# Optimization experiments

Measured on AMD Instinct MI355X. Metric: run time of the kernel, lower is better.

The kernel has to match this reference:

```python
import jax, jax.numpy as jnp
import numpy as np

N = 100000
E = 3200000
IN_DIM = 256
HID = 64
OUT = 40


def setup_inputs() -> dict:
    key = jax.random.key(0)
    ks = jax.random.split(key, 8)
    x = jax.random.normal(ks[0], (N, IN_DIM), dtype=jnp.float32)
    edge_index = jax.random.randint(ks[1], (2, E), 0, N, dtype=jnp.int64)
    # Glorot-ish init for weights
    W1 = jax.random.normal(ks[2], (IN_DIM, HID), dtype=jnp.float32) / np.sqrt(IN_DIM)
    b1 = jnp.zeros((HID,), dtype=jnp.float32)
    W2 = jax.random.normal(ks[3], (HID, HID), dtype=jnp.float32) / np.sqrt(HID)
    b2 = jnp.zeros((HID,), dtype=jnp.float32)
    W3 = jax.random.normal(ks[4], (HID, OUT), dtype=jnp.float32) / np.sqrt(HID)
    b3 = jax.random.normal(ks[5], (OUT,), dtype=jnp.float32) * 0.01
    return {"x": x, "edge_index": edge_index,
            "W1": W1, "b1": b1, "W2": W2, "b2": b2, "W3": W3, "b3": b3}


def _gcn_norm(edge_index, n):
    # Add self-loops, compute symmetric normalization deg^-1/2 A deg^-1/2
    loop = jnp.arange(n, dtype=edge_index.dtype)
    src = jnp.concatenate([edge_index[0], loop])
    dst = jnp.concatenate([edge_index[1], loop])
    deg = jax.ops.segment_sum(jnp.ones_like(dst, dtype=jnp.float32), dst,
                              num_segments=n)
    dinv = jnp.where(deg > 0, jax.lax.rsqrt(deg), 0.0)
    norm = dinv[src] * dinv[dst]  # [E+N]
    return src, dst, norm


def _gcn_conv(x, src, dst, norm, W, b, n):
    h = x @ W                                  # transform first (small dim)
    msg = h[src] * norm[:, None]               # gather + scale
    out = jax.ops.segment_sum(msg, dst, num_segments=n)  # scatter-add
    return out + b


def reference(x, edge_index, W1, b1, W2, b2, W3, b3):
    n = x.shape[0]
    src, dst, norm = _gcn_norm(edge_index, n)
    h = jax.nn.relu(_gcn_conv(x, src, dst, norm, W1, b1, n))
    h = jax.nn.relu(_gcn_conv(h, src, dst, norm, W2, b2, n))
    logits = h @ W3 + b3
    return jax.nn.log_softmax(logits, axis=1)
```

## Files before the change

kernel.cpp:

```cpp
#include <hip/hip_runtime.h>
#include <hip/hip_fp16.h>
#include <cstdint>


constexpr int CHUNK = 8192;
constexpr int BKCAP = 8192;

__global__ __launch_bounds__(256) void p2_localsort(
        const int* __restrict__ esrc, const int* __restrict__ edst, int E,
        unsigned* __restrict__ pairs1, int* __restrict__ cntMat,
        int* __restrict__ startMat, int NBK) {
    __shared__ int hist[1024];
    __shared__ int wsum[256];
    __shared__ unsigned lp[CHUNK];
    const int t = threadIdx.x, blk = blockIdx.x;
    const int base = blk * CHUNK;
    const int cnt = min(CHUNK, E - base);
    for (int i = t; i < 1024; i += 256) hist[i] = 0;
    __syncthreads();
    for (int i = t; i < cnt; i += 256) atomicAdd(&hist[edst[base + i] >> 7], 1);
    __syncthreads();
    int h0 = hist[4*t], h1 = hist[4*t+1], h2 = hist[4*t+2], h3 = hist[4*t+3];
    int s = h0 + h1 + h2 + h3;
    wsum[t] = s; __syncthreads();
    #pragma unroll
    for (int o = 1; o < 256; o <<= 1) {
        int x = (t >= o) ? wsum[t - o] : 0;
        __syncthreads(); wsum[t] += x; __syncthreads();
    }
    int run = wsum[t] - s;
    int e0 = run, e1 = run + h0, e2 = e1 + h1, e3 = e2 + h2;
    hist[4*t] = e0; hist[4*t+1] = e1; hist[4*t+2] = e2; hist[4*t+3] = e3;
    if (4*t     < NBK) { cntMat[(size_t)blk*NBK + 4*t]     = h0; startMat[(size_t)blk*NBK + 4*t]     = e0; }
    if (4*t + 1 < NBK) { cntMat[(size_t)blk*NBK + 4*t + 1] = h1; startMat[(size_t)blk*NBK + 4*t + 1] = e1; }
    if (4*t + 2 < NBK) { cntMat[(size_t)blk*NBK + 4*t + 2] = h2; startMat[(size_t)blk*NBK + 4*t + 2] = e2; }
    if (4*t + 3 < NBK) { cntMat[(size_t)blk*NBK + 4*t + 3] = h3; startMat[(size_t)blk*NBK + 4*t + 3] = e3; }
    __syncthreads();
    for (int i = t; i < cnt; i += 256) {
        int d = edst[base + i];
        int pos = atomicAdd(&hist[d >> 7], 1);
        lp[pos] = ((unsigned)(d & 127) << 17) | (unsigned)esrc[base + i];
    }
    __syncthreads();
    for (int i = t; i < cnt; i += 256) pairs1[base + i] = lp[i];
}

__global__ __launch_bounds__(256) void p3_colscan(int* __restrict__ cntMat,
        int* __restrict__ TB, int nchunks, int NBK) {
    __shared__ int buf[512];
    const int t = threadIdx.x, b = blockIdx.x;
    int v0 = (t < nchunks) ? cntMat[(size_t)t*NBK + b] : 0;
    int v1 = (t + 256 < nchunks) ? cntMat[(size_t)(t + 256)*NBK + b] : 0;
    buf[t] = v0; buf[t + 256] = v1; __syncthreads();
    #pragma unroll
    for (int o = 1; o < 512; o <<= 1) {
        int x0 = (t >= o) ? buf[t - o] : 0;
        int x1 = (t + 256 >= o) ? buf[t + 256 - o] : 0;
        __syncthreads(); buf[t] += x0; buf[t + 256] += x1; __syncthreads();
    }
    if (t < nchunks) cntMat[(size_t)t*NBK + b] = buf[t] - v0;
    if (t + 256 < nchunks) cntMat[(size_t)(t + 256)*NBK + b] = buf[t + 256] - v1;
    if (t == 0) TB[b] = buf[511];
}

__global__ __launch_bounds__(256) void p4_scan(const int* __restrict__ TB,
        int* __restrict__ bucketBase, int NBK, int E) {
    __shared__ int buf[1024];
    __shared__ int wsum[256];
    const int t = threadIdx.x;
    for (int i = t; i < 1024; i += 256) buf[i] = (i < NBK) ? TB[i] : 0;
    __syncthreads();
    int h0 = buf[4*t], h1 = buf[4*t+1], h2 = buf[4*t+2], h3 = buf[4*t+3];
    int s = h0 + h1 + h2 + h3;
    wsum[t] = s; __syncthreads();
    #pragma unroll
    for (int o = 1; o < 256; o <<= 1) {
        int x = (t >= o) ? wsum[t - o] : 0;
        __syncthreads(); wsum[t] += x; __syncthreads();
    }
    int run = wsum[t] - s;
    int e0 = run, e1 = run + h0, e2 = e1 + h1, e3 = e2 + h2;
    if (4*t     < NBK) bucketBase[4*t]     = e0;
    if (4*t + 1 < NBK) bucketBase[4*t + 1] = e1;
    if (4*t + 2 < NBK) bucketBase[4*t + 2] = e2;
    if (4*t + 3 < NBK) bucketBase[4*t + 3] = e3;
    if (t == 0) bucketBase[NBK] = E;
}

__global__ __launch_bounds__(256) void p6_sortcsr(
        const unsigned* __restrict__ pairs1, const int* __restrict__ cumMat,
        const int* __restrict__ startMat, const int* __restrict__ TB,
        const int* __restrict__ bucketBase, int nchunks, int NBK,
        int* __restrict__ csrc, int* __restrict__ rofs,
        float* __restrict__ dinv, int N, int E) {
    __shared__ unsigned lp[BKCAP];
    __shared__ int ccum[512];
    __shared__ int cstart[512];
    __shared__ int hist[128];
    __shared__ int sc[128];
    __shared__ int foffs[128];
    const int t = threadIdx.x, b = blockIdx.x;
    const int total0 = TB[b];
    const int total = min(total0, BKCAP);
    const int base = bucketBase[b];
    for (int i = t; i < nchunks; i += 256) {
        ccum[i]   = cumMat[(size_t)i * NBK + b];
        cstart[i] = startMat[(size_t)i * NBK + b];
    }
    if (t < 128) hist[t] = 0;
    if (t == 0) ccum[nchunks] = total0;
    __syncthreads();
    for (int i = t; i < total; i += 256) {
        int lo = 0, hi = nchunks - 1;
        while (lo < hi) {
            int mid = (lo + hi + 1) >> 1;
            if (ccum[mid] <= i) lo = mid; else hi = mid - 1;
        }
        unsigned v = pairs1[(size_t)lo * CHUNK + cstart[lo] + (i - ccum[lo])];
        lp[i] = v;
        atomicAdd(&hist[v >> 17], 1);
    }
    __syncthreads();
    if (t < 128) sc[t] = hist[t];
    __syncthreads();
    #pragma unroll
    for (int o = 1; o < 128; o <<= 1) {
        int x = (t >= o && t < 128) ? sc[t - o] : 0;
        __syncthreads();
        if (t < 128) sc[t] += x;
        __syncthreads();
    }
    if (t < 128) {
        int excl = sc[t] - hist[t];
        foffs[t] = excl;
        int node = b * 128 + t;
        if (node < N) {
            rofs[node] = base + excl;
            dinv[node] = rsqrtf((float)hist[t] + 1.0f);
        }
    }
    if (b == 0 && t == 255) rofs[N] = E;
    __syncthreads();
    for (int i = t; i < total; i += 256) {
        unsigned v = lp[i];
        int pos = atomicAdd(&foffs[v >> 17], 1);
        csrc[base + pos] = (int)(v & 0x1FFFFu);
    }
}

template<int K>
__global__ __launch_bounds__(256) void k_gemm(const float* __restrict__ X,
        const float* __restrict__ Wm, const float* __restrict__ dinv,
        __half* __restrict__ G, int nrows) {
    constexpr int BK = 32;
    constexpr int NCH = K / BK;
    constexpr int PITCH = 132;
    __shared__ float Xs[BK * PITCH];
    __shared__ float Ws[BK * 64];
    const int t = threadIdx.x;
    const int cg = t & 7;
    const int rg = t >> 3;
    const int brow = blockIdx.x * 128;

    float acc[4][8];
    #pragma unroll
    for (int r = 0; r < 4; ++r)
        #pragma unroll
        for (int c = 0; c < 8; ++c) acc[r][c] = 0.f;

    for (int ch = 0; ch < NCH; ++ch) {
        if (ch) __syncthreads();
        #pragma unroll
        for (int i = 0; i < 4; ++i) {
            int f = t + i * 256;
            int r = f >> 3, c4 = f & 7;
            int gr = brow + r;
            float4 v = make_float4(0.f, 0.f, 0.f, 0.f);
            if (gr < nrows)
                v = *(const float4*)(X + (size_t)gr * K + ch * BK + c4 * 4);
            Xs[(c4 * 4 + 0) * PITCH + r] = v.x;
            Xs[(c4 * 4 + 1) * PITCH + r] = v.y;
            Xs[(c4 * 4 + 2) * PITCH + r] = v.z;
            Xs[(c4 * 4 + 3) * PITCH + r] = v.w;
        }
        #pragma unroll
        for (int i = 0; i < 2; ++i) {
            int f = t + i * 256;
            int k = f >> 4, c4 = f & 15;
            *(float4*)(Ws + k * 64 + c4 * 4) =
                *(const float4*)(Wm + (size_t)(ch * BK + k) * 64 + c4 * 4);
        }
        __syncthreads();

        #pragma unroll
        for (int k = 0; k < BK; ++k) {
            float4 xa = *(const float4*)(Xs + k * PITCH + rg * 4);
            float4 w0 = *(const float4*)(Ws + k * 64 + cg * 8);
            float4 w1 = *(const float4*)(Ws + k * 64 + cg * 8 + 4);
#define FMA_ROW(r, xv) \
            acc[r][0] += (xv) * w0.x; acc[r][1] += (xv) * w0.y; \
            acc[r][2] += (xv) * w0.z; acc[r][3] += (xv) * w0.w; \
            acc[r][4] += (xv) * w1.x; acc[r][5] += (xv) * w1.y; \
            acc[r][6] += (xv) * w1.z; acc[r][7] += (xv) * w1.w;
            FMA_ROW(0, xa.x) FMA_ROW(1, xa.y) FMA_ROW(2, xa.z) FMA_ROW(3, xa.w)
#undef FMA_ROW
        }
    }
    #pragma unroll
    for (int r = 0; r < 4; ++r) {
        int gr = brow + rg * 4 + r;
        if (gr < nrows) {
            float dv = dinv[gr];
            __half2 h01 = __floats2half2_rn(acc[r][0] * dv, acc[r][1] * dv);
            __half2 h23 = __floats2half2_rn(acc[r][2] * dv, acc[r][3] * dv);
            __half2 h45 = __floats2half2_rn(acc[r][4] * dv, acc[r][5] * dv);
            __half2 h67 = __floats2half2_rn(acc[r][6] * dv, acc[r][7] * dv);
            uint4 pk;
            pk.x = *(unsigned*)&h01; pk.y = *(unsigned*)&h23;
            pk.z = *(unsigned*)&h45; pk.w = *(unsigned*)&h67;
            *(uint4*)(G + (size_t)gr * 64 + cg * 8) = pk;
        }
    }
}

#define ACC8(A0, A1, V) { \
    float2 f0_ = __half22float2(*(const __half2*)&(V).x); \
    float2 f1_ = __half22float2(*(const __half2*)&(V).y); \
    float2 f2_ = __half22float2(*(const __half2*)&(V).z); \
    float2 f3_ = __half22float2(*(const __half2*)&(V).w); \
    (A0).x += f0_.x; (A0).y += f0_.y; (A0).z += f1_.x; (A0).w += f1_.y; \
    (A1).x += f2_.x; (A1).y += f2_.y; (A1).z += f3_.x; (A1).w += f3_.y; }

__global__ __launch_bounds__(256) void k_agg(const __half* __restrict__ G,
        const int* __restrict__ rofs, const int* __restrict__ csrc,
        const float* __restrict__ dinv, const float* __restrict__ bias,
        float* __restrict__ H, int nrows) {
    const int l = threadIdx.x & 63;
    const int g = l >> 3;
    const int p = l & 7;
    const int d = blockIdx.x * 4 + (threadIdx.x >> 6);
    if (d >= nrows) return;
    const int beg = rofs[d], end = rofs[d + 1];
    float4 a0 = make_float4(0.f, 0.f, 0.f, 0.f);
    float4 a1 = make_float4(0.f, 0.f, 0.f, 0.f);

    int e = beg + g;
    for (; e + 8 < end; e += 16) {
        int s0 = csrc[e];
        int s1 = csrc[e + 8];
        uint4 v0 = *(const uint4*)(G + (size_t)s0 * 64 + p * 8);
        uint4 v1 = *(const uint4*)(G + (size_t)s1 * 64 + p * 8);
        ACC8(a0, a1, v0)
        ACC8(a0, a1, v1)
    }
    if (e < end) {
        int s = csrc[e];
        uint4 v = *(const uint4*)(G + (size_t)s * 64 + p * 8);
        ACC8(a0, a1, v)
    }
    #pragma unroll
    for (int off = 8; off <= 32; off <<= 1) {
        a0.x += __shfl_xor(a0.x, off); a0.y += __shfl_xor(a0.y, off);
        a0.z += __shfl_xor(a0.z, off); a0.w += __shfl_xor(a0.w, off);
        a1.x += __shfl_xor(a1.x, off); a1.y += __shfl_xor(a1.y, off);
        a1.z += __shfl_xor(a1.z, off); a1.w += __shfl_xor(a1.w, off);
    }
    if (g == 0) {
        uint4 sv = *(const uint4*)(G + (size_t)d * 64 + p * 8);
        float2 s0 = __half22float2(*(const __half2*)&sv.x);
        float2 s1 = __half22float2(*(const __half2*)&sv.y);
        float2 s2 = __half22float2(*(const __half2*)&sv.z);
        float2 s3 = __half22float2(*(const __half2*)&sv.w);
        const float dv = dinv[d];
        const float4* B4 = (const float4*)bias;
        float4 b0 = B4[p * 2], b1 = B4[p * 2 + 1];
        float4 o0, o1;
        o0.x = fmaxf((a0.x + s0.x) * dv + b0.x, 0.f);
        o0.y = fmaxf((a0.y + s0.y) * dv + b0.y, 0.f);
        o0.z = fmaxf((a0.z + s1.x) * dv + b0.z, 0.f);
        o0.w = fmaxf((a0.w + s1.y) * dv + b0.w, 0.f);
        o1.x = fmaxf((a1.x + s2.x) * dv + b1.x, 0.f);
        o1.y = fmaxf((a1.y + s2.y) * dv + b1.y, 0.f);
        o1.z = fmaxf((a1.z + s3.x) * dv + b1.z, 0.f);
        o1.w = fmaxf((a1.w + s3.y) * dv + b1.w, 0.f);
        float4* H4 = (float4*)(H + (size_t)d * 64 + p * 8);
        H4[0] = o0; H4[1] = o1;
    }
}

__global__ __launch_bounds__(256) void k_final(const float* __restrict__ H,
        const float* __restrict__ W3, const float* __restrict__ b3,
        float* __restrict__ out, int nrows) {
    constexpr int HP = 68;
    constexpr int OP = 44;
    __shared__ float wl[64 * 40];
    __shared__ float bl[40];
    __shared__ float Hs[256 * HP];
    const int t = threadIdx.x;
    for (int i = t; i < 640; i += 256)
        ((float4*)wl)[i] = ((const float4*)W3)[i];
    if (t < 40) bl[t] = b3[t];
    const int brow = blockIdx.x * 256;
    const int rows = min(256, nrows - brow);
    for (int i = t; i < rows * 16; i += 256) {
        int r = i >> 4, c = i & 15;
        float4 v = ((const float4*)(H + (size_t)(brow + r) * 64))[c];
        *(float4*)&Hs[r * HP + c * 4] = v;
    }
    __syncthreads();

    float acc[40];
    float lse = 0.f;
    if (t < rows) {
        #pragma unroll
        for (int j = 0; j < 40; ++j) acc[j] = bl[j];
        #pragma unroll
        for (int k4 = 0; k4 < 16; ++k4) {
            float4 h4 = *(const float4*)&Hs[t * HP + k4 * 4];
            float hv[4] = {h4.x, h4.y, h4.z, h4.w};
            #pragma unroll
            for (int c = 0; c < 4; ++c) {
                const float4* wr = (const float4*)(wl + (k4 * 4 + c) * 40);
                #pragma unroll
                for (int j4 = 0; j4 < 10; ++j4) {
                    float4 wv = wr[j4];
                    acc[j4 * 4 + 0] += hv[c] * wv.x;
                    acc[j4 * 4 + 1] += hv[c] * wv.y;
                    acc[j4 * 4 + 2] += hv[c] * wv.z;
                    acc[j4 * 4 + 3] += hv[c] * wv.w;
                }
            }
        }
        float m = acc[0];
        #pragma unroll
        for (int j = 1; j < 40; ++j) m = fmaxf(m, acc[j]);
        float s = 0.f;
        #pragma unroll
        for (int j = 0; j < 40; ++j) s += expf(acc[j] - m);
        lse = m + logf(s);
    }
    __syncthreads();
    float* Os = Hs;
    if (t < rows) {
        #pragma unroll
        for (int j4 = 0; j4 < 10; ++j4)
            *(float4*)&Os[t * OP + j4 * 4] =
                make_float4(acc[j4 * 4 + 0] - lse, acc[j4 * 4 + 1] - lse,
                            acc[j4 * 4 + 2] - lse, acc[j4 * 4 + 3] - lse);
    }
    __syncthreads();
    for (int i = t; i < rows * 40; i += 256) {
        int r = i / 40, c = i - r * 40;
        out[(size_t)brow * 40 + i] = Os[r * OP + c];
    }
}

extern "C" void kernel_launch(void* const* d_in, const int* in_sizes, int n_in,
                              void* d_out, int out_size, void* d_ws, size_t ws_size,
                              hipStream_t stream) {
    const float* x  = (const float*)d_in[0];
    const int*   ei = (const int*)d_in[1];
    const float* W1 = (const float*)d_in[2];
    const float* b1 = (const float*)d_in[3];
    const float* W2 = (const float*)d_in[4];
    const float* b2 = (const float*)d_in[5];
    const float* W3 = (const float*)d_in[6];
    const float* b3 = (const float*)d_in[7];
    float* out = (float*)d_out;

    const int HID = in_sizes[3];
    const int IND = in_sizes[2] / HID;
    const int N   = in_sizes[0] / IND;
    const int E   = in_sizes[1] / 2;
    (void)HID; (void)n_in; (void)out_size; (void)ws_size;

    const int NBK     = (N + 127) >> 7;
    const int nchunks = (E + CHUNK - 1) / CHUNK;

    char* ws = (char*)d_ws;
    size_t off = 0;
    auto alloc = [&](size_t bytes) -> char* {
        char* p = ws + off;
        off = (off + bytes + 255) & ~(size_t)255;
        return p;
    };
    size_t gbytes = (size_t)N * 64 * 2;
    size_t p1bytes = (size_t)E * 4;
    int*      cntMat     = (int*)     alloc((size_t)nchunks * NBK * 4);
    int*      startMat   = (int*)     alloc((size_t)nchunks * NBK * 4);
    int*      TB         = (int*)     alloc((size_t)NBK * 4);
    int*      bucketBase = (int*)     alloc(((size_t)NBK + 1) * 4);
    float*    dinv       = (float*)   alloc((size_t)N * 4);
    int*      rofs       = (int*)     alloc(((size_t)N + 1) * 4);
    int*      csrc       = (int*)     alloc((size_t)E * 4);
    __half*   g          = (__half*)  alloc(gbytes > p1bytes ? gbytes : p1bytes);
    float*    h          = (float*)   alloc((size_t)N * 64 * 4);
    unsigned* pairs1     = (unsigned*)g;

    const int* esrc = ei;
    const int* edst = ei + E;
    const int gM = (N + 127) / 128;
    const int gN = (N + 255) / 256;

    p2_localsort<<<nchunks, 256, 0, stream>>>(esrc, edst, E, pairs1, cntMat, startMat, NBK);
    p3_colscan  <<<NBK, 256, 0, stream>>>(cntMat, TB, nchunks, NBK);
    p4_scan     <<<1, 256, 0, stream>>>(TB, bucketBase, NBK, E);
    p6_sortcsr  <<<NBK, 256, 0, stream>>>(pairs1, cntMat, startMat, TB, bucketBase,
                                          nchunks, NBK, csrc, rofs, dinv, N, E);

    k_gemm<256> <<<gM, 256, 0, stream>>>(x, W1, dinv, g, N);
    k_agg       <<<(N + 3) / 4, 256, 0, stream>>>(g, rofs, csrc, dinv, b1, h, N);
    k_gemm<64>  <<<gM, 256, 0, stream>>>(h, W2, dinv, g, N);
    k_agg       <<<(N + 3) / 4, 256, 0, stream>>>(g, rofs, csrc, dinv, b2, h, N);
    k_final     <<<gN, 256, 0, stream>>>(h, W3, b3, out, N);
}
```

Baseline: 291.8 us.

## Restructure GEMM tile to 512 threads, 2 rows per thread, row-major LDS

Reworks the node-feature GEMM to use 512-thread blocks, each thread computing 2 rows by 8 columns instead of 4 by 8. The K chunk grows from 32 to 64, and X is stored row-major in LDS with a 65-float pitch instead of being transposed. The aim is more waves for latency hiding, fewer barriers per chunk and cheaper LDS stores. In exchange there is less register reuse per thread (2 rows per W load) and scalar LDS reads of X in place of float4 loads.

Result: slower. 306.2 us (+4.9%).

```diff
diff --git a/kernel.cpp b/kernel.cpp
--- a/kernel.cpp
+++ b/kernel.cpp
@@ -149,22 +149,22 @@
 }
 
 template<int K>
-__global__ __launch_bounds__(256) void k_gemm(const float* __restrict__ X,
+__global__ __launch_bounds__(512) void k_gemm(const float* __restrict__ X,
         const float* __restrict__ Wm, const float* __restrict__ dinv,
         __half* __restrict__ G, int nrows) {
-    constexpr int BK = 32;
+    constexpr int BK = 64;
     constexpr int NCH = K / BK;
-    constexpr int PITCH = 132;
-    __shared__ float Xs[BK * PITCH];
+    constexpr int XP = 65;
+    __shared__ float Xs[128 * XP];
     __shared__ float Ws[BK * 64];
     const int t = threadIdx.x;
     const int cg = t & 7;
     const int rg = t >> 3;
     const int brow = blockIdx.x * 128;
 
-    float acc[4][8];
-    #pragma unroll
-    for (int r = 0; r < 4; ++r)
+    float acc[2][8];
+    #pragma unroll
+    for (int r = 0; r < 2; ++r)
         #pragma unroll
         for (int c = 0; c < 8; ++c) acc[r][c] = 0.f;
 
@@ -172,43 +172,45 @@
         if (ch) __syncthreads();
         #pragma unroll
         for (int i = 0; i < 4; ++i) {
-            int f = t + i * 256;
-            int r = f >> 3, c4 = f & 7;
+            int f = t + i * 512;
+            int r = f >> 4, c4 = f & 15;
             int gr = brow + r;
             float4 v = make_float4(0.f, 0.f, 0.f, 0.f);
             if (gr < nrows)
                 v = *(const float4*)(X + (size_t)gr * K + ch * BK + c4 * 4);
-            Xs[(c4 * 4 + 0) * PITCH + r] = v.x;
-            Xs[(c4 * 4 + 1) * PITCH + r] = v.y;
-            Xs[(c4 * 4 + 2) * PITCH + r] = v.z;
-            Xs[(c4 * 4 + 3) * PITCH + r] = v.w;
+            float* xr = Xs + r * XP + c4 * 4;
+            xr[0] = v.x; xr[1] = v.y; xr[2] = v.z; xr[3] = v.w;
         }
         #pragma unroll
         for (int i = 0; i < 2; ++i) {
-            int f = t + i * 256;
+            int f = t + i * 512;
             int k = f >> 4, c4 = f & 15;
             *(float4*)(Ws + k * 64 + c4 * 4) =
                 *(const float4*)(Wm + (size_t)(ch * BK + k) * 64 + c4 * 4);
         }
         __syncthreads();
 
-        #pragma unroll
+        const float* x0p = Xs + (rg * 2 + 0) * XP;
+        const float* x1p = Xs + (rg * 2 + 1) * XP;
+        #pragma unroll 8
         for (int k = 0; k < BK; ++k) {
-            float4 xa = *(const float4*)(Xs + k * PITCH + rg * 4);
+            float x0 = x0p[k];
+            float x1 = x1p[k];
             float4 w0 = *(const float4*)(Ws + k * 64 + cg * 8);
             float4 w1 = *(const float4*)(Ws + k * 64 + cg * 8 + 4);
-#define FMA_ROW(r, xv) \
-            acc[r][0] += (xv) * w0.x; acc[r][1] += (xv) * w0.y; \
-            acc[r][2] += (xv) * w0.z; acc[r][3] += (xv) * w0.w; \
-            acc[r][4] += (xv) * w1.x; acc[r][5] += (xv) * w1.y; \
-            acc[r][6] += (xv) * w1.z; acc[r][7] += (xv) * w1.w;
-            FMA_ROW(0, xa.x) FMA_ROW(1, xa.y) FMA_ROW(2, xa.z) FMA_ROW(3, xa.w)
-#undef FMA_ROW
-        }
-    }
-    #pragma unroll
-    for (int r = 0; r < 4; ++r) {
-        int gr = brow + rg * 4 + r;
+            acc[0][0] += x0 * w0.x; acc[0][1] += x0 * w0.y;
+            acc[0][2] += x0 * w0.z; acc[0][3] += x0 * w0.w;
+            acc[0][4] += x0 * w1.x; acc[0][5] += x0 * w1.y;
+            acc[0][6] += x0 * w1.z; acc[0][7] += x0 * w1.w;
+            acc[1][0] += x1 * w0.x; acc[1][1] += x1 * w0.y;
+            acc[1][2] += x1 * w0.z; acc[1][3] += x1 * w0.w;
+            acc[1][4] += x1 * w1.x; acc[1][5] += x1 * w1.y;
+            acc[1][6] += x1 * w1.z; acc[1][7] += x1 * w1.w;
+        }
+    }
+    #pragma unroll
+    for (int r = 0; r < 2; ++r) {
+        int gr = brow + rg * 2 + r;
         if (gr < nrows) {
             float dv = dinv[gr];
             __half2 h01 = __floats2half2_rn(acc[r][0] * dv, acc[r][1] * dv);
@@ -408,9 +410,9 @@
     p6_sortcsr  <<<NBK, 256, 0, stream>>>(pairs1, cntMat, startMat, TB, bucketBase,
                                           nchunks, NBK, csrc, rofs, dinv, N, E);
 
-    k_gemm<256> <<<gM, 256, 0, stream>>>(x, W1, dinv, g, N);
+    k_gemm<256> <<<gM, 512, 0, stream>>>(x, W1, dinv, g, N);
     k_agg       <<<(N + 3) / 4, 256, 0, stream>>>(g, rofs, csrc, dinv, b1, h, N);
-    k_gemm<64>  <<<gM, 256, 0, stream>>>(h, W2, dinv, g, N);
+    k_gemm<64>  <<<gM, 512, 0, stream>>>(h, W2, dinv, g, N);
     k_agg       <<<(N + 3) / 4, 256, 0, stream>>>(g, rofs, csrc, dinv, b2, h, N);
     k_final     <<<gN, 256, 0, stream>>>(h, W3, b3, out, N);
 }
```

## Shrink GEMM tile to 64 rows with 4x4 microtile and XOR-swizzled LDS

Applied to the files above, without the earlier changes.

The dense transform kernel now processes 64 rows per block instead of 128, with each thread computing a 4x4 output microtile rather than 4x8. The transposed X tile in shared memory uses an XOR swizzle on the row index instead of padding, to avoid bank conflicts on the transposed stores. This doubles the grid size and reduces registers and shared memory per block, aiming for better occupancy and more blocks across CUs. The cost is lower arithmetic intensity per LDS load and narrower output stores.

Result: no change. 289.5 us (-0.8%).

```diff
diff --git a/kernel.cpp b/kernel.cpp
--- a/kernel.cpp
+++ b/kernel.cpp
@@ -154,34 +154,35 @@
         __half* __restrict__ G, int nrows) {
     constexpr int BK = 32;
     constexpr int NCH = K / BK;
-    constexpr int PITCH = 132;
-    __shared__ float Xs[BK * PITCH];
+    constexpr int XP = 68;
+    __shared__ float Xs[BK * XP];
     __shared__ float Ws[BK * 64];
     const int t = threadIdx.x;
-    const int cg = t & 7;
-    const int rg = t >> 3;
-    const int brow = blockIdx.x * 128;
-
-    float acc[4][8];
+    const int cg = t & 15;
+    const int rg = t >> 4;
+    const int brow = blockIdx.x * 64;
+
+    float acc[4][4];
     #pragma unroll
     for (int r = 0; r < 4; ++r)
         #pragma unroll
-        for (int c = 0; c < 8; ++c) acc[r][c] = 0.f;
+        for (int c = 0; c < 4; ++c) acc[r][c] = 0.f;
 
     for (int ch = 0; ch < NCH; ++ch) {
         if (ch) __syncthreads();
         #pragma unroll
-        for (int i = 0; i < 4; ++i) {
+        for (int i = 0; i < 2; ++i) {
             int f = t + i * 256;
             int r = f >> 3, c4 = f & 7;
             int gr = brow + r;
             float4 v = make_float4(0.f, 0.f, 0.f, 0.f);
             if (gr < nrows)
                 v = *(const float4*)(X + (size_t)gr * K + ch * BK + c4 * 4);
-            Xs[(c4 * 4 + 0) * PITCH + r] = v.x;
-            Xs[(c4 * 4 + 1) * PITCH + r] = v.y;
-            Xs[(c4 * 4 + 2) * PITCH + r] = v.z;
-            Xs[(c4 * 4 + 3) * PITCH + r] = v.w;
+            int rsw = r ^ (c4 << 2);
+            Xs[(c4 * 4 + 0) * XP + rsw] = v.x;
+            Xs[(c4 * 4 + 1) * XP + rsw] = v.y;
+            Xs[(c4 * 4 + 2) * XP + rsw] = v.z;
+            Xs[(c4 * 4 + 3) * XP + rsw] = v.w;
         }
         #pragma unroll
         for (int i = 0; i < 2; ++i) {
@@ -194,16 +195,17 @@
 
         #pragma unroll
         for (int k = 0; k < BK; ++k) {
-            float4 xa = *(const float4*)(Xs + k * PITCH + rg * 4);
-            float4 w0 = *(const float4*)(Ws + k * 64 + cg * 8);
-            float4 w1 = *(const float4*)(Ws + k * 64 + cg * 8 + 4);
-#define FMA_ROW(r, xv) \
-            acc[r][0] += (xv) * w0.x; acc[r][1] += (xv) * w0.y; \
-            acc[r][2] += (xv) * w0.z; acc[r][3] += (xv) * w0.w; \
-            acc[r][4] += (xv) * w1.x; acc[r][5] += (xv) * w1.y; \
-            acc[r][6] += (xv) * w1.z; acc[r][7] += (xv) * w1.w;
-            FMA_ROW(0, xa.x) FMA_ROW(1, xa.y) FMA_ROW(2, xa.z) FMA_ROW(3, xa.w)
-#undef FMA_ROW
+            const int xsw = (k >> 2) << 2;
+            float4 xa = *(const float4*)(Xs + k * XP + ((rg * 4) ^ xsw));
+            float4 wv = *(const float4*)(Ws + k * 64 + cg * 4);
+            acc[0][0] += xa.x * wv.x; acc[0][1] += xa.x * wv.y;
+            acc[0][2] += xa.x * wv.z; acc[0][3] += xa.x * wv.w;
+            acc[1][0] += xa.y * wv.x; acc[1][1] += xa.y * wv.y;
+            acc[1][2] += xa.y * wv.z; acc[1][3] += xa.y * wv.w;
+            acc[2][0] += xa.z * wv.x; acc[2][1] += xa.z * wv.y;
+            acc[2][2] += xa.z * wv.z; acc[2][3] += xa.z * wv.w;
+            acc[3][0] += xa.w * wv.x; acc[3][1] += xa.w * wv.y;
+            acc[3][2] += xa.w * wv.z; acc[3][3] += xa.w * wv.w;
         }
     }
     #pragma unroll
@@ -213,12 +215,9 @@
             float dv = dinv[gr];
             __half2 h01 = __floats2half2_rn(acc[r][0] * dv, acc[r][1] * dv);
             __half2 h23 = __floats2half2_rn(acc[r][2] * dv, acc[r][3] * dv);
-            __half2 h45 = __floats2half2_rn(acc[r][4] * dv, acc[r][5] * dv);
-            __half2 h67 = __floats2half2_rn(acc[r][6] * dv, acc[r][7] * dv);
-            uint4 pk;
+            uint2 pk;
             pk.x = *(unsigned*)&h01; pk.y = *(unsigned*)&h23;
-            pk.z = *(unsigned*)&h45; pk.w = *(unsigned*)&h67;
-            *(uint4*)(G + (size_t)gr * 64 + cg * 8) = pk;
+            *(uint2*)(G + (size_t)gr * 64 + cg * 4) = pk;
         }
     }
 }
@@ -399,7 +398,7 @@
 
     const int* esrc = ei;
     const int* edst = ei + E;
-    const int gM = (N + 127) / 128;
+    const int gM = (N + 63) / 64;
     const int gN = (N + 255) / 256;
 
     p2_localsort<<<nchunks, 256, 0, stream>>>(esrc, edst, E, pairs1, cntMat, startMat, NBK);
```
